# Kernel optimization log

Hardware: AMD Instinct MI355X
Metric: run time of the kernel (lower is better)

The kernel has to match this reference:

```python
import jax, jax.numpy as jnp
import numpy as np

B_POINTS = 1024   # batch of independent spatial points
NF = 672          # hourly forcing samples (28 days * 24 h)

def setup_inputs() -> dict:
    key = jax.random.key(0)
    k1, k2, k3 = jax.random.split(key, 3)
    # pk ~ [-10, -9] as in the source, with small perturbation
    pk = jnp.array([-10.0, -9.0], jnp.float32) + 0.1 * jax.random.normal(k1, (2,), jnp.float32)
    # wind stress ~ O(0.1) N/m^2
    TAx = 0.1 * jax.random.normal(k2, (B_POINTS, NF), jnp.float32)
    TAy = 0.1 * jax.random.normal(k3, (B_POINTS, NF), jnp.float32)
    fc = jnp.float32(1e-4)  # Coriolis frequency
    return {"pk": pk, "TAx": TAx, "TAy": TAy, "fc": fc,
            "nt": 40320, "dt": 60, "dt_forcing": 3600}

def reference(pk, TAx, TAy, fc, nt, dt, dt_forcing):
    # Slab-ocean 1D model, explicit Euler (difx=True branch of the source):
    #   dU/dt =  fc*V + K0*TAx(t) - K1*U
    #   dV/dt = -fc*U + K0*TAy(t) - K1*V
    # with TAx/TAy linearly interpolated from hourly forcing to the dt grid.
    K = jnp.exp(pk)                       # [2]
    nsub = dt_forcing // dt               # substeps per forcing sample (60)
    nf = TAx.shape[-1]                    # number of forcing samples
    dtf = jnp.float32(dt)

    def step(carry, it):
        U, V = carry                      # [B], [B]
        itf = it // nsub
        aa = (jnp.mod(it, nsub) / nsub).astype(jnp.float32)
        itsup = jnp.where(itf + 1 >= nf, nf - 1, itf + 1)
        tax = (1.0 - aa) * TAx[:, itf] + aa * TAx[:, itsup]
        tay = (1.0 - aa) * TAy[:, itf] + aa * TAy[:, itsup]
        Un = U + dtf * ( fc * V + K[0] * tax - K[1] * U)
        Vn = V + dtf * (-fc * U + K[0] * tay - K[1] * V)
        return (Un, Vn), Un

    B = TAx.shape[0]
    U0 = jnp.zeros((B,), jnp.float32)
    _, Us = jax.lax.scan(step, (U0, U0), jnp.arange(nt, dtype=jnp.int32))
    return Us  # [nt, B] zonal velocity saved after each Euler step
```

## Files before the change

### kernel.cpp

```cpp
#include <hip/hip_runtime.h>


#define NT    40320
#define BPTS  1024
#define NF    672
#define NSUB  60
#define CH    60
#define NCH   (NT / CH)
#define PPT   4
#define NW    36
#define NV    (NW / 4)
#define TP    256
#define NTILE (BPTS / TP)

typedef float vf4 __attribute__((ext_vector_type(4)));

__global__ __launch_bounds__(256, 2)
void slab_chunk(const float* __restrict__ pk,
                const float* __restrict__ TAx,
                const float* __restrict__ TAy,
                const float* __restrict__ fcp,
                const int* __restrict__ dtp,
                float* __restrict__ out) {
    const int k   = blockIdx.x;
    const int tid = threadIdx.x;

    const float dtf = (float)dtp[0];
    const float K0  = expf(pk[0]);
    const float K1  = expf(pk[1]);
    const float ar  = 1.0f - dtf * K1;
    const float ai  = -dtf * fcp[0];
    const float bs  = dtf * K0;

    float g1r = 0.f, g1i = 0.f, g2r = 0.f, g2i = 0.f;
    float pr = 1.f, pi = 0.f;
    for (int m = 0; m < NSUB; ++m) {
        g1r += pr; g1i += pi;
        float w = (float)(NSUB - 1 - m) * (1.0f / NSUB);
        g2r = fmaf(w, pr, g2r); g2i = fmaf(w, pi, g2i);
        float nr = pr * ar - pi * ai;
        float ni = pr * ai + pi * ar;
        pr = nr; pi = ni;
    }
    const float Ar  = pr,        Ai  = pi;
    const float cAr = g1r - g2r, cAi = g1i - g2i;
    const float cBr = g2r,       cBi = g2i;
    const float cCr = cAr + (Ar * cBr - Ai * cBi);
    const float cCi = cAi + (Ar * cBi + Ai * cBr);

    int va = (k + 4) & ~3;
    if (va > NF) va = NF;
    const int ja = va - NW;

    float wgtR[NW], wgtI[NW];
    {
        float Wr = 1.f, Wi = 0.f;
#pragma unroll
        for (int i = NW - 1; i >= 0; --i) {
            const int m = ja + i;
            float er = 0.f, ei = 0.f;
            if (k > 0 && m >= 0 && m <= k) {
                if (m == k) { er = cBr; ei = cBi; }
                else {
                    const float br = (m == 0) ? cAr : cCr;
                    const float bi = (m == 0) ? cAi : cCi;
                    er = Wr * br - Wi * bi;
                    ei = Wr * bi + Wi * br;
                    const float t2 = Wr * Ar - Wi * Ai;
                    Wi = Wr * Ai + Wi * Ar; Wr = t2;
                }
            }
            wgtR[i] = er; wgtI[i] = ei;
        }
    }

    __shared__ float ldsx[TP][NW];
    __shared__ float ldsy[TP][NW];
    float zr4[NTILE], zi4[NTILE];

#pragma unroll
    for (int tau = 0; tau < NTILE; ++tau) {
#pragma unroll
        for (int it = 0; it < NV; ++it) {
            const int V = tid + 256 * it;
            const int r = V / NV;
            const int v = V - r * NV;
            int off = ja + 4 * v; if (off < 0) off = 0;
            const size_t gbase = (size_t)(tau * TP + r) * NF + off;
            *(vf4*)&ldsx[r][4 * v] = *(const vf4*)(TAx + gbase);
            *(vf4*)&ldsy[r][4 * v] = *(const vf4*)(TAy + gbase);
        }
        __syncthreads();

        float aR = 0.f, aI = 0.f;
#pragma unroll
        for (int v = 0; v < NV; ++v) {
            const vf4 fx = *(const vf4*)&ldsx[tid][4 * v];
            const vf4 fy = *(const vf4*)&ldsy[tid][4 * v];
#pragma unroll
            for (int e = 0; e < 4; ++e) {
                const int i = 4 * v + e;
                aR = fmaf(wgtR[i], fx[e], fmaf(-wgtI[i], fy[e], aR));
                aI = fmaf(wgtR[i], fy[e], fmaf( wgtI[i], fx[e], aI));
            }
        }
        zr4[tau] = bs * aR; zi4[tau] = bs * aI;
        __syncthreads();
    }

    float2* zbuf = (float2*)&ldsx[0][0];
#pragma unroll
    for (int tau = 0; tau < NTILE; ++tau)
        zbuf[tau * TP + tid] = make_float2(zr4[tau], zi4[tau]);
    __syncthreads();

    const int p0 = tid * PPT;
    float zr[PPT], zi[PPT];
#pragma unroll
    for (int j = 0; j < PPT; ++j) {
        float2 z = zbuf[p0 + j];
        zr[j] = z.x; zi[j] = z.y;
    }

    const int f0 = k;
    const int f1 = (k + 1 < NF) ? k + 1 : NF - 1;

    float bx[PPT], by[PPT], dbx[PPT], dby[PPT];
#pragma unroll
    for (int j = 0; j < PPT; ++j) {
        const float* rx = TAx + (size_t)(p0 + j) * NF;
        const float* ry = TAy + (size_t)(p0 + j) * NF;
        const float x0 = rx[f0], x1 = rx[f1];
        const float y0 = ry[f0], y1 = ry[f1];
        bx[j]  = bs * x0;
        by[j]  = bs * y0;
        dbx[j] = bs * (x1 - x0) * (1.0f / NSUB);
        dby[j] = bs * (y1 - y0) * (1.0f / NSUB);
    }

    float* orow = out + (size_t)k * CH * BPTS + p0;

#pragma unroll 10
    for (int s = 0; s < CH; ++s) {
#pragma unroll
        for (int j = 0; j < PPT; ++j) {
            const float ur = fmaf(ar, zr[j], fmaf(-ai, zi[j], bx[j]));
            const float vi = fmaf(ar, zi[j], fmaf( ai, zr[j], by[j]));
            zr[j] = ur; zi[j] = vi;
            bx[j] += dbx[j]; by[j] += dby[j];
        }
        vf4 v; v.x = zr[0]; v.y = zr[1]; v.z = zr[2]; v.w = zr[3];
        __builtin_nontemporal_store(v, (vf4*)orow);
        orow += BPTS;
    }
}

extern "C" void kernel_launch(void* const* d_in, const int* in_sizes, int n_in,
                              void* d_out, int out_size, void* d_ws, size_t ws_size,
                              hipStream_t stream) {
    const float* pk  = (const float*)d_in[0];
    const float* TAx = (const float*)d_in[1];
    const float* TAy = (const float*)d_in[2];
    const float* fcp = (const float*)d_in[3];
    const int*   dtp = (const int*)d_in[5];
    float* out = (float*)d_out;

    slab_chunk<<<NCH, 256, 0, stream>>>(pk, TAx, TAy, fcp, dtp, out);
}
```

Baseline: 56.40 us.

## Halve LDS footprint by staging TAx and TAy separately, hoist forcing loads

Replaces the two LDS staging arrays with a single one that holds TAx and then TAy in two passes, and recombines the complex dot product algebraically. This halves shared memory per block so the launch bound can ask for 3 blocks per CU. It also hoists the per-point forcing-endpoint loads to the kernel start so their latency overlaps the weight setup, and it replaces the nontemporal output stores with plain stores. In exchange it adds two extra barriers per tile and puts more register pressure under the tighter launch bound.

```diff
diff --git a/kernel.cpp b/kernel.cpp
--- a/kernel.cpp
+++ b/kernel.cpp
@@ -15,7 +15,7 @@
 
 typedef float vf4 __attribute__((ext_vector_type(4)));
 
-__global__ __launch_bounds__(256, 2)
+__global__ __launch_bounds__(256, 3)
 void slab_chunk(const float* __restrict__ pk,
                 const float* __restrict__ TAx,
                 const float* __restrict__ TAy,
@@ -31,6 +31,18 @@
     const float ar  = 1.0f - dtf * K1;
     const float ai  = -dtf * fcp[0];
     const float bs  = dtf * K0;
+
+    const int p0 = tid * PPT;
+    const int f0 = k;
+    const int f1 = (k + 1 < NF) ? k + 1 : NF - 1;
+    float x0[PPT], x1[PPT], y0[PPT], y1[PPT];
+#pragma unroll
+    for (int j = 0; j < PPT; ++j) {
+        const float* rx = TAx + (size_t)(p0 + j) * NF;
+        const float* ry = TAy + (size_t)(p0 + j) * NF;
+        x0[j] = rx[f0]; x1[j] = rx[f1];
+        y0[j] = ry[f0]; y1[j] = ry[f1];
+    }
 
     float g1r = 0.f, g1i = 0.f, g2r = 0.f, g2i = 0.f;
     float pr = 1.f, pi = 0.f;
@@ -74,47 +86,74 @@
         }
     }
 
-    __shared__ float ldsx[TP][NW];
-    __shared__ float ldsy[TP][NW];
+    __shared__ float lds[TP][NW];
     float zr4[NTILE], zi4[NTILE];
 
 #pragma unroll
     for (int tau = 0; tau < NTILE; ++tau) {
+        float aR = 0.f, aI = 0.f;
+
 #pragma unroll
         for (int it = 0; it < NV; ++it) {
             const int V = tid + 256 * it;
             const int r = V / NV;
             const int v = V - r * NV;
             int off = ja + 4 * v; if (off < 0) off = 0;
-            const size_t gbase = (size_t)(tau * TP + r) * NF + off;
-            *(vf4*)&ldsx[r][4 * v] = *(const vf4*)(TAx + gbase);
-            *(vf4*)&ldsy[r][4 * v] = *(const vf4*)(TAy + gbase);
-        }
-        __syncthreads();
-
-        float aR = 0.f, aI = 0.f;
-#pragma unroll
-        for (int v = 0; v < NV; ++v) {
-            const vf4 fx = *(const vf4*)&ldsx[tid][4 * v];
-            const vf4 fy = *(const vf4*)&ldsy[tid][4 * v];
-#pragma unroll
-            for (int e = 0; e < 4; ++e) {
-                const int i = 4 * v + e;
-                aR = fmaf(wgtR[i], fx[e], fmaf(-wgtI[i], fy[e], aR));
-                aI = fmaf(wgtR[i], fy[e], fmaf( wgtI[i], fx[e], aI));
+            *(vf4*)&lds[r][4 * v] =
+                *(const vf4*)(TAx + (size_t)(tau * TP + r) * NF + off);
+        }
+        __syncthreads();
+        {
+            float dR = 0.f, dI = 0.f;
+#pragma unroll
+            for (int v = 0; v < NV; ++v) {
+                const vf4 f = *(const vf4*)&lds[tid][4 * v];
+#pragma unroll
+                for (int e = 0; e < 4; ++e) {
+                    const int i = 4 * v + e;
+                    dR = fmaf(wgtR[i], f[e], dR);
+                    dI = fmaf(wgtI[i], f[e], dI);
+                }
             }
-        }
+            aR += dR; aI += dI;
+        }
+        __syncthreads();
+
+#pragma unroll
+        for (int it = 0; it < NV; ++it) {
+            const int V = tid + 256 * it;
+            const int r = V / NV;
+            const int v = V - r * NV;
+            int off = ja + 4 * v; if (off < 0) off = 0;
+            *(vf4*)&lds[r][4 * v] =
+                *(const vf4*)(TAy + (size_t)(tau * TP + r) * NF + off);
+        }
+        __syncthreads();
+        {
+            float dR = 0.f, dI = 0.f;
+#pragma unroll
+            for (int v = 0; v < NV; ++v) {
+                const vf4 f = *(const vf4*)&lds[tid][4 * v];
+#pragma unroll
+                for (int e = 0; e < 4; ++e) {
+                    const int i = 4 * v + e;
+                    dR = fmaf(wgtR[i], f[e], dR);
+                    dI = fmaf(wgtI[i], f[e], dI);
+                }
+            }
+            aR -= dI; aI += dR;
+        }
+        __syncthreads();
+
         zr4[tau] = bs * aR; zi4[tau] = bs * aI;
-        __syncthreads();
-    }
-
-    float2* zbuf = (float2*)&ldsx[0][0];
+    }
+
+    float2* zbuf = (float2*)&lds[0][0];
 #pragma unroll
     for (int tau = 0; tau < NTILE; ++tau)
         zbuf[tau * TP + tid] = make_float2(zr4[tau], zi4[tau]);
     __syncthreads();
 
-    const int p0 = tid * PPT;
     float zr[PPT], zi[PPT];
 #pragma unroll
     for (int j = 0; j < PPT; ++j) {
@@ -122,20 +161,13 @@
         zr[j] = z.x; zi[j] = z.y;
     }
 
-    const int f0 = k;
-    const int f1 = (k + 1 < NF) ? k + 1 : NF - 1;
-
     float bx[PPT], by[PPT], dbx[PPT], dby[PPT];
 #pragma unroll
     for (int j = 0; j < PPT; ++j) {
-        const float* rx = TAx + (size_t)(p0 + j) * NF;
-        const float* ry = TAy + (size_t)(p0 + j) * NF;
-        const float x0 = rx[f0], x1 = rx[f1];
-        const float y0 = ry[f0], y1 = ry[f1];
-        bx[j]  = bs * x0;
-        by[j]  = bs * y0;
-        dbx[j] = bs * (x1 - x0) * (1.0f / NSUB);
-        dby[j] = bs * (y1 - y0) * (1.0f / NSUB);
+        bx[j]  = bs * x0[j];
+        by[j]  = bs * y0[j];
+        dbx[j] = bs * (x1[j] - x0[j]) * (1.0f / NSUB);
+        dby[j] = bs * (y1[j] - y0[j]) * (1.0f / NSUB);
     }
 
     float* orow = out + (size_t)k * CH * BPTS + p0;
@@ -150,7 +182,7 @@
             bx[j] += dbx[j]; by[j] += dby[j];
         }
         vf4 v; v.x = zr[0]; v.y = zr[1]; v.z = zr[2]; v.w = zr[3];
-        __builtin_nontemporal_store(v, (vf4*)orow);
+        *(vf4*)orow = v;
         orow += BPTS;
     }
 }
```

Result: slower. 67.82 us (+20.3%).

## Process two forcing chunks per block with async LDS loads and XCD remap

Applied to the files above, without the earlier changes.

Each block now computes two consecutive forcing chunks, so it runs one warm-start weighted sum over the history window (now 32 taps instead of 36) and then marches 120 Euler steps. The grid is halved and the block index is remapped across the 8 XCDs. History tiles are loaded with global_load_lds straight into LDS using an XOR swizzle to avoid bank conflicts. The goal is to amortize the per-block warm-start gather, at the cost of a longer serial march per block, fewer blocks, and a smaller window that relies on the decay of A^m to stay accurate.

```diff
diff --git a/kernel.cpp b/kernel.cpp
--- a/kernel.cpp
+++ b/kernel.cpp
@@ -7,13 +7,22 @@
 #define NSUB  60
 #define CH    60
 #define NCH   (NT / CH)
+#define CG    2
+#define NPAIR (NCH / CG)
 #define PPT   4
-#define NW    36
+#define NW    32
 #define NV    (NW / 4)
 #define TP    256
 #define NTILE (BPTS / TP)
+#define NXCD  8
 
 typedef float vf4 __attribute__((ext_vector_type(4)));
+
+__device__ __forceinline__ void gload_lds16(const float* g, float* l) {
+    __builtin_amdgcn_global_load_lds(
+        (const __attribute__((address_space(1))) void*)g,
+        (__attribute__((address_space(3))) void*)l, 16, 0, 0);
+}
 
 __global__ __launch_bounds__(256, 2)
 void slab_chunk(const float* __restrict__ pk,
@@ -22,7 +31,9 @@
                 const float* __restrict__ fcp,
                 const int* __restrict__ dtp,
                 float* __restrict__ out) {
-    const int k   = blockIdx.x;
+    const int bid = blockIdx.x;
+    const int kp  = (bid & (NXCD - 1)) * (NPAIR / NXCD) + (bid >> 3);
+    const int k0  = kp * CG;
     const int tid = threadIdx.x;
 
     const float dtf = (float)dtp[0];
@@ -48,7 +59,7 @@
     const float cCr = cAr + (Ar * cBr - Ai * cBi);
     const float cCi = cAi + (Ar * cBi + Ai * cBr);
 
-    int va = (k + 4) & ~3;
+    int va = (k0 + 4) & ~3;
     if (va > NF) va = NF;
     const int ja = va - NW;
 
@@ -59,8 +70,8 @@
         for (int i = NW - 1; i >= 0; --i) {
             const int m = ja + i;
             float er = 0.f, ei = 0.f;
-            if (k > 0 && m >= 0 && m <= k) {
-                if (m == k) { er = cBr; ei = cBi; }
+            if (k0 > 0 && m >= 0 && m <= k0) {
+                if (m == k0) { er = cBr; ei = cBi; }
                 else {
                     const float br = (m == 0) ? cAr : cCr;
                     const float bi = (m == 0) ? cAi : cCi;
@@ -82,21 +93,23 @@
     for (int tau = 0; tau < NTILE; ++tau) {
 #pragma unroll
         for (int it = 0; it < NV; ++it) {
-            const int V = tid + 256 * it;
-            const int r = V / NV;
-            const int v = V - r * NV;
-            int off = ja + 4 * v; if (off < 0) off = 0;
-            const size_t gbase = (size_t)(tau * TP + r) * NF + off;
-            *(vf4*)&ldsx[r][4 * v] = *(const vf4*)(TAx + gbase);
-            *(vf4*)&ldsy[r][4 * v] = *(const vf4*)(TAy + gbase);
+            const int V  = tid + 256 * it;
+            const int r  = V >> 3;
+            const int u  = V & 7;
+            const int uu = u ^ (r & 7);
+            int off = ja + 4 * uu; if (off < 0) off = 0;
+            const size_t gb = (size_t)(tau * TP + r) * NF + off;
+            gload_lds16(TAx + gb, &ldsx[0][0] + (size_t)V * 4);
+            gload_lds16(TAy + gb, &ldsy[0][0] + (size_t)V * 4);
         }
         __syncthreads();
 
         float aR = 0.f, aI = 0.f;
 #pragma unroll
         for (int v = 0; v < NV; ++v) {
-            const vf4 fx = *(const vf4*)&ldsx[tid][4 * v];
-            const vf4 fy = *(const vf4*)&ldsy[tid][4 * v];
+            const int sv = v ^ (tid & 7);
+            const vf4 fx = *(const vf4*)&ldsx[tid][4 * sv];
+            const vf4 fy = *(const vf4*)&ldsy[tid][4 * sv];
 #pragma unroll
             for (int e = 0; e < 4; ++e) {
                 const int i = 4 * v + e;
@@ -122,36 +135,46 @@
         zr[j] = z.x; zi[j] = z.y;
     }
 
-    const int f0 = k;
-    const int f1 = (k + 1 < NF) ? k + 1 : NF - 1;
-
-    float bx[PPT], by[PPT], dbx[PPT], dby[PPT];
+    float x0[PPT], y0[PPT];
 #pragma unroll
     for (int j = 0; j < PPT; ++j) {
-        const float* rx = TAx + (size_t)(p0 + j) * NF;
-        const float* ry = TAy + (size_t)(p0 + j) * NF;
-        const float x0 = rx[f0], x1 = rx[f1];
-        const float y0 = ry[f0], y1 = ry[f1];
-        bx[j]  = bs * x0;
-        by[j]  = bs * y0;
-        dbx[j] = bs * (x1 - x0) * (1.0f / NSUB);
-        dby[j] = bs * (y1 - y0) * (1.0f / NSUB);
+        x0[j] = TAx[(size_t)(p0 + j) * NF + k0];
+        y0[j] = TAy[(size_t)(p0 + j) * NF + k0];
     }
 
-    float* orow = out + (size_t)k * CH * BPTS + p0;
+    float* orow = out + (size_t)k0 * CH * BPTS + p0;
+
+    for (int c = 0; c < CG; ++c) {
+        const int kk = k0 + c;
+        const int f1 = (kk + 1 < NF) ? kk + 1 : NF - 1;
+
+        float x1[PPT], y1[PPT], bx[PPT], by[PPT], dbx[PPT], dby[PPT];
+#pragma unroll
+        for (int j = 0; j < PPT; ++j) {
+            x1[j] = TAx[(size_t)(p0 + j) * NF + f1];
+            y1[j] = TAy[(size_t)(p0 + j) * NF + f1];
+            bx[j]  = bs * x0[j];
+            by[j]  = bs * y0[j];
+            dbx[j] = bs * (x1[j] - x0[j]) * (1.0f / NSUB);
+            dby[j] = bs * (y1[j] - y0[j]) * (1.0f / NSUB);
+        }
 
 #pragma unroll 10
-    for (int s = 0; s < CH; ++s) {
+        for (int s = 0; s < CH; ++s) {
 #pragma unroll
-        for (int j = 0; j < PPT; ++j) {
-            const float ur = fmaf(ar, zr[j], fmaf(-ai, zi[j], bx[j]));
-            const float vi = fmaf(ar, zi[j], fmaf( ai, zr[j], by[j]));
-            zr[j] = ur; zi[j] = vi;
-            bx[j] += dbx[j]; by[j] += dby[j];
+            for (int j = 0; j < PPT; ++j) {
+                const float ur = fmaf(ar, zr[j], fmaf(-ai, zi[j], bx[j]));
+                const float vi = fmaf(ar, zi[j], fmaf( ai, zr[j], by[j]));
+                zr[j] = ur; zi[j] = vi;
+                bx[j] += dbx[j]; by[j] += dby[j];
+            }
+            vf4 v; v.x = zr[0]; v.y = zr[1]; v.z = zr[2]; v.w = zr[3];
+            __builtin_nontemporal_store(v, (vf4*)orow);
+            orow += BPTS;
         }
-        vf4 v; v.x = zr[0]; v.y = zr[1]; v.z = zr[2]; v.w = zr[3];
-        __builtin_nontemporal_store(v, (vf4*)orow);
-        orow += BPTS;
+
+#pragma unroll
+        for (int j = 0; j < PPT; ++j) { x0[j] = x1[j]; y0[j] = y1[j]; }
     }
 }
 
@@ -165,5 +188,5 @@
     const int*   dtp = (const int*)d_in[5];
     float* out = (float*)d_out;
 
-    slab_chunk<<<NCH, 256, 0, stream>>>(pk, TAx, TAy, fcp, dtp, out);
+    slab_chunk<<<NPAIR, 256, 0, stream>>>(pk, TAx, TAy, fcp, dtp, out);
 }
```

After: 49.01 us. 13.1% less time.
